# Kernel optimization log

Measured on AMD Instinct MI355X. Metric: run time of the kernel, lower is better.

## Reference

```python
import jax, jax.numpy as jnp
import numpy as np

EPS = 1e-12  # torch F.normalize eps


def setup_inputs() -> dict:
    key = jax.random.key(0)
    k1, k2, k3, k4, k5 = jax.random.split(key, 5)
    N, C, H, W = 32, 512, 32, 32
    E = 1024   # expansion * dim
    G = 8      # group
    D = E // G # 128, per-group channel dim
    K = 64     # num_clusters
    x = jax.random.normal(k1, (N, C, H, W), dtype=jnp.float32)
    W1 = jax.random.normal(k2, (E, C), dtype=jnp.float32) / np.sqrt(C)
    W2 = jax.random.normal(k3, (G, E), dtype=jnp.float32) / np.sqrt(E)
    Wc = jax.random.normal(k4, (K, D), dtype=jnp.float32) / np.sqrt(D)
    centroids = jax.random.uniform(k5, (K, D), dtype=jnp.float32)
    return {"x": x, "W1": W1, "W2": W2, "Wc": Wc, "centroids": centroids}


def reference(x, W1, W2, Wc, centroids):
    # x: [N, C, H, W]; W1: [E, C]; W2: [G, E]; Wc: [K, D]; centroids: [K, D]
    N, C, H, W = x.shape
    E = W1.shape[0]
    G = W2.shape[0]
    K, D = Wc.shape
    P = H * W
    # descriptor-wise L2 normalization over channel dim
    norm = jnp.linalg.norm(x, axis=1, keepdims=True)
    x = x / jnp.maximum(norm, EPS)
    # linear1 on channels: [N, E, P]
    xe = jnp.einsum('ncp,ec->nep', x.reshape(N, C, P), W1)
    # grouped features: [N, G, D, P]
    xg = xe.reshape(N, G, D, P)
    # attention gate: sigmoid(linear2)  -> [N, G, P]
    att = jax.nn.sigmoid(jnp.einsum('nep,ge->ngp', xe, W2))
    # 1x1 conv = per-pixel matmul with cluster weights -> [N, G, K, P]
    soft_assign = jax.nn.softmax(jnp.einsum('ngdp,kd->ngkp', xg, Wc), axis=2)
    # combined per-(cluster,pixel) weight
    w = soft_assign * att[:, :, None, :]  # [N, G, K, P]
    # NetVLAD residual aggregation, algebraically decomposed to avoid the
    # giant [N,G,K,D,P] intermediate:
    #   vlad[n,k,d] = sum_{g,p} w * xg  -  centroids[k,d] * sum_{g,p} w
    agg = jnp.einsum('ngkp,ngdp->nkd', w, xg)  # [N, K, D]
    wsum = w.sum(axis=(1, 3))                  # [N, K]
    vlad = agg - wsum[:, :, None] * centroids[None]  # [N, K, D]
    return vlad.reshape(N, K * D)
```

## Files before the change

### kernel.cpp

```cpp
#include <hip/hip_runtime.h>


#define N_  32
#define C_  512
#define P_  1024
#define E_  1024
#define G_  8
#define D_  128
#define K_  64

typedef __attribute__((ext_vector_type(8))) short bf16x8;
typedef __attribute__((ext_vector_type(4))) float f32x4;

__device__ __forceinline__ unsigned short f2b(float f) {
    union { float f; unsigned u; } v; v.f = f;
    unsigned r = (v.u + 0x7FFFu + ((v.u >> 16) & 1u)) >> 16;
    return (unsigned short)r;
}
__device__ __forceinline__ float b2f(unsigned short h) {
    union { unsigned u; float f; } v; v.u = ((unsigned)h) << 16;
    return v.f;
}

__device__ __forceinline__ void gl_lds16(const void* g, void* l) {
    __builtin_amdgcn_global_load_lds(
        (const __attribute__((address_space(1))) void*)g,
        (__attribute__((address_space(3))) void*)l, 16, 0, 0);
}

__global__ __launch_bounds__(256) void k1_norm_prep(const float* __restrict__ x,
                                                    const float* __restrict__ W1,
                                                    const float* __restrict__ Wc,
                                                    unsigned short* __restrict__ xhat_t,
                                                    unsigned short* __restrict__ W1b,
                                                    unsigned short* __restrict__ Vb) {
    __shared__ short xc[128 * 256];
    __shared__ float red[256];
    __shared__ float rn[64];
    int t = threadIdx.x;

    if (blockIdx.x >= 16) {
        int bid = (blockIdx.x - 16) * 32 + blockIdx.y;
        int i0 = bid * 512 + t;
        W1b[i0]       = f2b(W1[i0]);
        W1b[i0 + 256] = f2b(W1[i0 + 256]);
        int ch = bid & 1, k = (bid >> 1) & 63, g = bid >> 7;
        int c = ch * 256 + t;
        float acc = 0.f;
        #pragma unroll 8
        for (int d = 0; d < 128; ++d)
            acc += Wc[k * 128 + d] * W1[(g * 128 + d) * C_ + c];
        Vb[(g * 64 + k) * C_ + c] = f2b(acc);
        return;
    }

    int n = blockIdx.y;
    int p0 = blockIdx.x * 64;
    int ps = t & 63, cs = t >> 6;

    float ss = 0.f;
    for (int i = 0; i < 128; ++i) {
        float v = x[((size_t)(n * C_ + cs * 128 + i)) * P_ + p0 + ps];
        ss += v * v;
        xc[i * 256 + t] = (short)f2b(v);
    }
    red[t] = ss;
    __syncthreads();
    if (t < 64) {
        float s = red[t] + red[64 + t] + red[128 + t] + red[192 + t];
        rn[t] = 1.0f / fmaxf(sqrtf(s), 1e-12f);
    }
    __syncthreads();

    float r = rn[ps];
    size_t base = ((size_t)(n * P_ + p0 + ps)) * C_ + cs * 128;
    #pragma unroll
    for (int jj = 0; jj < 16; ++jj) {
        bf16x8 o;
        #pragma unroll
        for (int j = 0; j < 8; ++j)
            o[j] = (short)f2b(b2f((unsigned short)xc[(jj * 8 + j) * 256 + t]) * r);
        *(bf16x8*)&xhat_t[base + jj * 8] = o;
    }
}

__global__ __launch_bounds__(256) void k2_gemm_xe(const unsigned short* __restrict__ W1b,
                                                  const unsigned short* __restrict__ xhat_t,
                                                  unsigned short* __restrict__ xe) {
    __shared__ __align__(16) short As[128 * 32];
    __shared__ __align__(16) short Bs[128 * 32];
    int n = blockIdx.y;
    int e0 = (blockIdx.x >> 3) * 128;
    int p0 = (blockIdx.x & 7) * 128;
    int t = threadIdx.x;
    int w = t >> 6, l = t & 63, q = l >> 4, l15 = l & 15;
    int wr = w >> 1, wc = w & 1;

    f32x4 acc[4][4];
    #pragma unroll
    for (int mi = 0; mi < 4; ++mi)
        #pragma unroll
        for (int ni = 0; ni < 4; ++ni)
            acc[mi][ni] = (f32x4){0.f, 0.f, 0.f, 0.f};

    for (int ks = 0; ks < 16; ++ks) {
        int k0 = ks * 32;
        #pragma unroll
        for (int i = 0; i < 2; ++i) {
            int ch = i * 256 + t;
            int row = ch >> 2, col = (ch & 3) * 8;
            gl_lds16(&W1b[(e0 + row) * C_ + k0 + col], &As[ch * 8]);
        }
        #pragma unroll
        for (int i = 0; i < 2; ++i) {
            int ch = i * 256 + t;
            int row = ch >> 2, col = (ch & 3) * 8;
            gl_lds16(&xhat_t[((size_t)(n * P_ + p0 + row)) * C_ + k0 + col], &Bs[ch * 8]);
        }
        __syncthreads();

        bf16x8 af[4], bf[4];
        #pragma unroll
        for (int mi = 0; mi < 4; ++mi)
            af[mi] = *(const bf16x8*)&As[(wr * 64 + mi * 16 + l15) * 32 + q * 8];
        #pragma unroll
        for (int ni = 0; ni < 4; ++ni)
            bf[ni] = *(const bf16x8*)&Bs[(wc * 64 + ni * 16 + l15) * 32 + q * 8];
        #pragma unroll
        for (int mi = 0; mi < 4; ++mi)
            #pragma unroll
            for (int ni = 0; ni < 4; ++ni)
                acc[mi][ni] = __builtin_amdgcn_mfma_f32_16x16x32_bf16(af[mi], bf[ni], acc[mi][ni], 0, 0, 0);
        __syncthreads();
    }

    #pragma unroll
    for (int mi = 0; mi < 4; ++mi) {
        #pragma unroll
        for (int ni = 0; ni < 4; ++ni) {
            #pragma unroll
            for (int r = 0; r < 4; ++r) {
                int e = e0 + wr * 64 + mi * 16 + q * 4 + r;
                int p = p0 + wc * 64 + ni * 16 + l15;
                xe[((size_t)(n * E_ + e)) * P_ + p] = f2b(acc[mi][ni][r]);
            }
        }
    }
}

__global__ __launch_bounds__(256) void k3a_att_part(const unsigned short* __restrict__ xe,
                                                    const float* __restrict__ W2,
                                                    float* __restrict__ att_part) {
    int n = blockIdx.y;
    int ec = blockIdx.x;
    int t = threadIdx.x;
    int e0 = ec * 64;
    f32x4 acc[8];
    #pragma unroll
    for (int g = 0; g < 8; ++g) acc[g] = (f32x4){0.f, 0.f, 0.f, 0.f};
    #pragma unroll 4
    for (int i = 0; i < 64; ++i) {
        int e = e0 + i;
        ushort4 v4 = *(const ushort4*)&xe[((size_t)(n * E_ + e)) * P_ + t * 4];
        f32x4 vf = {b2f(v4.x), b2f(v4.y), b2f(v4.z), b2f(v4.w)};
        #pragma unroll
        for (int g = 0; g < 8; ++g)
            acc[g] += vf * W2[g * E_ + e];
    }
    #pragma unroll
    for (int g = 0; g < 8; ++g)
        *(f32x4*)&att_part[(((size_t)(n * 16 + ec)) * 8 + g) * P_ + t * 4] = acc[g];
}

__global__ __launch_bounds__(256) void k3b_att_reduce(const float* __restrict__ att_part,
                                                      float* __restrict__ att_s) {
    int idx = blockIdx.x * 256 + threadIdx.x;
    int p = idx & 1023;
    int g = (idx >> 10) & 7;
    int n = idx >> 13;
    float s = 0.f;
    #pragma unroll
    for (int ec = 0; ec < 16; ++ec)
        s += att_part[(((size_t)(n * 16 + ec)) * 8 + g) * P_ + p];
    att_s[idx] = 1.0f / (1.0f + __expf(-s));
}

__global__ __launch_bounds__(256) void k4_assign_agg(const unsigned short* __restrict__ Vb,
                                                     const unsigned short* __restrict__ xhat_t,
                                                     const unsigned short* __restrict__ xe,
                                                     const float* __restrict__ att_s,
                                                     float* __restrict__ agg_part,
                                                     float* __restrict__ wsum_part) {
    __shared__ __align__(16) char smem[34816 + 17408];
    short* xglds = (short*)smem;
    short* As2   = (short*)smem;
    short* Bs2   = (short*)(smem + 4096);
    short* wlds  = (short*)(smem + 34816);

    int g = blockIdx.x & 7, ph = blockIdx.x >> 3, n = blockIdx.y;
    int t = threadIdx.x;
    int w = t >> 6, l = t & 63, q = l >> 4, l15 = l & 15;

    f32x4 acc_a[4][2];
    #pragma unroll
    for (int mi = 0; mi < 4; ++mi)
        #pragma unroll
        for (int ni = 0; ni < 2; ++ni)
            acc_a[mi][ni] = (f32x4){0.f, 0.f, 0.f, 0.f};
    float wsp[16];
    #pragma unroll
    for (int j = 0; j < 16; ++j) wsp[j] = 0.f;

    for (int cc = 0; cc < 4; ++cc) {
        int p0c = ph * 512 + cc * 128;

        f32x4 acc_s[4][2];
        #pragma unroll
        for (int mi = 0; mi < 4; ++mi)
            #pragma unroll
            for (int ni = 0; ni < 2; ++ni)
                acc_s[mi][ni] = (f32x4){0.f, 0.f, 0.f, 0.f};

        for (int ks = 0; ks < 16; ++ks) {
            int k0 = ks * 32;
            {
                int row = t >> 2, col = (t & 3) * 8;
                gl_lds16(&Vb[(g * 64 + row) * C_ + k0 + col], &As2[t * 8]);
            }
            #pragma unroll
            for (int i = 0; i < 2; ++i) {
                int ch = i * 256 + t;
                int row = ch >> 2, col = (ch & 3) * 8;
                gl_lds16(&xhat_t[((size_t)(n * P_ + p0c + row)) * C_ + k0 + col], &Bs2[ch * 8]);
            }
            __syncthreads();
            bf16x8 af[4], bf2[2];
            #pragma unroll
            for (int mi = 0; mi < 4; ++mi)
                af[mi] = *(const bf16x8*)&As2[(mi * 16 + l15) * 32 + q * 8];
            #pragma unroll
            for (int ni = 0; ni < 2; ++ni)
                bf2[ni] = *(const bf16x8*)&Bs2[(w * 32 + ni * 16 + l15) * 32 + q * 8];
            #pragma unroll
            for (int mi = 0; mi < 4; ++mi)
                #pragma unroll
                for (int ni = 0; ni < 2; ++ni)
                    acc_s[mi][ni] = __builtin_amdgcn_mfma_f32_16x16x32_bf16(af[mi], bf2[ni], acc_s[mi][ni], 0, 0, 0);
            __syncthreads();
        }

        #pragma unroll
        for (int ni = 0; ni < 2; ++ni) {
            float m = -1e30f;
            #pragma unroll
            for (int mi = 0; mi < 4; ++mi)
                #pragma unroll
                for (int r = 0; r < 4; ++r)
                    m = fmaxf(m, acc_s[mi][ni][r]);
            m = fmaxf(m, __shfl_xor(m, 16));
            m = fmaxf(m, __shfl_xor(m, 32));
            float s = 0.f;
            #pragma unroll
            for (int mi = 0; mi < 4; ++mi)
                #pragma unroll
                for (int r = 0; r < 4; ++r) {
                    float e = __expf(acc_s[mi][ni][r] - m);
                    acc_s[mi][ni][r] = e;
                    s += e;
                }
            s += __shfl_xor(s, 16);
            s += __shfl_xor(s, 32);

            int pcol = p0c + w * 32 + ni * 16 + l15;
            float av = att_s[(((size_t)(n * G_ + g)) * P_) + pcol];
            float scale = av / s;

            #pragma unroll
            for (int mi = 0; mi < 4; ++mi)
                #pragma unroll
                for (int r = 0; r < 4; ++r) {
                    float wv = acc_s[mi][ni][r] * scale;
                    wsp[mi * 4 + r] += wv;
                    wlds[(mi * 16 + q * 4 + r) * 136 + (w * 32 + ni * 16 + l15)] = (short)f2b(wv);
                }
        }

        #pragma unroll
        for (int i = 0; i < 8; ++i) {
            int ch = i * 256 + t;
            int row = ch / 17, col = (ch % 17) * 8;
            gl_lds16(&xe[((size_t)(n * E_ + g * 128 + row)) * P_ + p0c + col], &xglds[ch * 8]);
        }
        if (t < 128) {
            int ch = 2048 + t;
            int row = ch / 17, col = (ch % 17) * 8;
            gl_lds16(&xe[((size_t)(n * E_ + g * 128 + row)) * P_ + p0c + col], &xglds[ch * 8]);
        }
        __syncthreads();

        #pragma unroll
        for (int pk = 0; pk < 4; ++pk) {
            bf16x8 a2[4], b2[2];
            #pragma unroll
            for (int mi = 0; mi < 4; ++mi)
                a2[mi] = *(const bf16x8*)&wlds[(mi * 16 + l15) * 136 + pk * 32 + q * 8];
            #pragma unroll
            for (int ni = 0; ni < 2; ++ni)
                b2[ni] = *(const bf16x8*)&xglds[(w * 32 + ni * 16 + l15) * 136 + pk * 32 + q * 8];
            #pragma unroll
            for (int mi = 0; mi < 4; ++mi)
                #pragma unroll
                for (int ni = 0; ni < 2; ++ni)
                    acc_a[mi][ni] = __builtin_amdgcn_mfma_f32_16x16x32_bf16(a2[mi], b2[ni], acc_a[mi][ni], 0, 0, 0);
        }
        __syncthreads();
    }

    size_t base = (((size_t)(n * G_ + g)) * 2 + ph) * 64;
    #pragma unroll
    for (int mi = 0; mi < 4; ++mi)
        #pragma unroll
        for (int ni = 0; ni < 2; ++ni)
            #pragma unroll
            for (int r = 0; r < 4; ++r) {
                int k = mi * 16 + q * 4 + r;
                int d = w * 32 + ni * 16 + l15;
                agg_part[(base + k) * 128 + d] = acc_a[mi][ni][r];
            }

    #pragma unroll
    for (int j = 0; j < 16; ++j) {
        float v = wsp[j];
        v += __shfl_xor(v, 1);
        v += __shfl_xor(v, 2);
        v += __shfl_xor(v, 4);
        v += __shfl_xor(v, 8);
        if (l15 == 0) {
            int k = (j >> 2) * 16 + q * 4 + (j & 3);
            wsum_part[((((size_t)(n * G_ + g)) * 2 + ph) * 4 + w) * 64 + k] = v;
        }
    }
}

__global__ __launch_bounds__(256) void k5_final(const float* __restrict__ agg_part,
                                                const float* __restrict__ wsum_part,
                                                const float* __restrict__ centroids,
                                                float* __restrict__ out) {
    int idx = blockIdx.x * 256 + threadIdx.x;
    int d = idx & 127;
    int k = (idx >> 7) & 63;
    int n = idx >> 13;
    float ws = 0.f;
    #pragma unroll
    for (int g = 0; g < 8; ++g)
        #pragma unroll
        for (int ph = 0; ph < 2; ++ph)
            #pragma unroll
            for (int w2 = 0; w2 < 4; ++w2)
                ws += wsum_part[((((size_t)(n * G_ + g)) * 2 + ph) * 4 + w2) * 64 + k];
    float agg = 0.f;
    #pragma unroll
    for (int g = 0; g < 8; ++g)
        #pragma unroll
        for (int ph = 0; ph < 2; ++ph)
            agg += agg_part[(((((size_t)(n * G_ + g)) * 2 + ph) * 64) + k) * 128 + d];
    out[idx] = agg - ws * centroids[k * 128 + d];
}

extern "C" void kernel_launch(void* const* d_in, const int* in_sizes, int n_in,
                              void* d_out, int out_size, void* d_ws, size_t ws_size,
                              hipStream_t stream) {
    const float* x         = (const float*)d_in[0];
    const float* W1        = (const float*)d_in[1];
    const float* W2        = (const float*)d_in[2];
    const float* Wc        = (const float*)d_in[3];
    const float* centroids = (const float*)d_in[4];
    float* out = (float*)d_out;

    char* ws = (char*)d_ws;
    unsigned short* W1b      = (unsigned short*)(ws + 0);
    unsigned short* Vb       = (unsigned short*)(ws + 1048576);
    unsigned short* xhat_t   = (unsigned short*)(ws + 1572864);
    unsigned short* xe       = (unsigned short*)(ws + 35127296);
    float*          att_s    = (float*)(ws + 102236160);
    float*          att_part = (float*)(ws + 103284736);
    float*          agg_part = (float*)(ws + 103284736);
    float*          wsum_part= (float*)(ws + 120061952);

    hipLaunchKernelGGL(k1_norm_prep,   dim3(48, 32), dim3(256), 0, stream,
                       x, W1, Wc, xhat_t, W1b, Vb);
    hipLaunchKernelGGL(k2_gemm_xe,     dim3(64, 32), dim3(256), 0, stream, W1b, xhat_t, xe);
    hipLaunchKernelGGL(k3a_att_part,   dim3(16, 32), dim3(256), 0, stream, xe, W2, att_part);
    hipLaunchKernelGGL(k3b_att_reduce, dim3(1024), dim3(256), 0, stream, att_part, att_s);
    hipLaunchKernelGGL(k4_assign_agg,  dim3(16, 32), dim3(256), 0, stream, Vb, xhat_t, xe,
                       att_s, agg_part, wsum_part);
    hipLaunchKernelGGL(k5_final,       dim3(1024), dim3(256), 0, stream,
                       agg_part, wsum_part, centroids, out);
}
```

Baseline: 262.7 us.

## Double K-step width in GEMMs, prefetch xe early, split prep kernel

The GEMM k2 and the assignment GEMM in k4 now stage 64-wide K slices per iteration instead of 32, which halves the number of barrier pairs and global-to-LDS rounds. In k4 the xe tile load is issued at the start of each pixel chunk into its own LDS region, so it overlaps the score GEMM and softmax instead of running after them. The weight prep (W1 cast and the Vb product) moves into a separate kernel so the normalization kernel no longer carries divergent block roles. In exchange LDS use per block grows, especially in k4, which may lower occupancy, and there is one extra kernel launch.

```diff
diff --git a/kernel.cpp b/kernel.cpp
--- a/kernel.cpp
+++ b/kernel.cpp
@@ -28,34 +28,32 @@
         (__attribute__((address_space(3))) void*)l, 16, 0, 0);
 }
 
-__global__ __launch_bounds__(256) void k1_norm_prep(const float* __restrict__ x,
-                                                    const float* __restrict__ W1,
-                                                    const float* __restrict__ Wc,
-                                                    unsigned short* __restrict__ xhat_t,
-                                                    unsigned short* __restrict__ W1b,
-                                                    unsigned short* __restrict__ Vb) {
+__global__ __launch_bounds__(256) void k0_prep(const float* __restrict__ W1,
+                                               const float* __restrict__ Wc,
+                                               unsigned short* __restrict__ W1b,
+                                               unsigned short* __restrict__ Vb) {
+    int bid = blockIdx.x;
+    int t = threadIdx.x;
+    int i0 = bid * 512 + t;
+    W1b[i0]       = f2b(W1[i0]);
+    W1b[i0 + 256] = f2b(W1[i0 + 256]);
+    int ch = bid & 1, k = (bid >> 1) & 63, g = bid >> 7;
+    int c = ch * 256 + t;
+    float acc = 0.f;
+    #pragma unroll 8
+    for (int d = 0; d < 128; ++d)
+        acc += Wc[k * 128 + d] * W1[(g * 128 + d) * C_ + c];
+    Vb[(g * 64 + k) * C_ + c] = f2b(acc);
+}
+
+__global__ __launch_bounds__(256) void k1_norm_transpose(const float* __restrict__ x,
+                                                         unsigned short* __restrict__ xhat_t) {
     __shared__ short xc[128 * 256];
     __shared__ float red[256];
     __shared__ float rn[64];
-    int t = threadIdx.x;
-
-    if (blockIdx.x >= 16) {
-        int bid = (blockIdx.x - 16) * 32 + blockIdx.y;
-        int i0 = bid * 512 + t;
-        W1b[i0]       = f2b(W1[i0]);
-        W1b[i0 + 256] = f2b(W1[i0 + 256]);
-        int ch = bid & 1, k = (bid >> 1) & 63, g = bid >> 7;
-        int c = ch * 256 + t;
-        float acc = 0.f;
-        #pragma unroll 8
-        for (int d = 0; d < 128; ++d)
-            acc += Wc[k * 128 + d] * W1[(g * 128 + d) * C_ + c];
-        Vb[(g * 64 + k) * C_ + c] = f2b(acc);
-        return;
-    }
-
     int n = blockIdx.y;
     int p0 = blockIdx.x * 64;
+    int t = threadIdx.x;
     int ps = t & 63, cs = t >> 6;
 
     float ss = 0.f;
@@ -87,8 +85,8 @@
 __global__ __launch_bounds__(256) void k2_gemm_xe(const unsigned short* __restrict__ W1b,
                                                   const unsigned short* __restrict__ xhat_t,
                                                   unsigned short* __restrict__ xe) {
-    __shared__ __align__(16) short As[128 * 32];
-    __shared__ __align__(16) short Bs[128 * 32];
+    __shared__ __align__(16) short As[128 * 64];
+    __shared__ __align__(16) short Bs[128 * 64];
     int n = blockIdx.y;
     int e0 = (blockIdx.x >> 3) * 128;
     int p0 = (blockIdx.x & 7) * 128;
@@ -103,34 +101,37 @@
         for (int ni = 0; ni < 4; ++ni)
             acc[mi][ni] = (f32x4){0.f, 0.f, 0.f, 0.f};
 
-    for (int ks = 0; ks < 16; ++ks) {
-        int k0 = ks * 32;
-        #pragma unroll
-        for (int i = 0; i < 2; ++i) {
+    for (int ks = 0; ks < 8; ++ks) {
+        int k0 = ks * 64;
+        #pragma unroll
+        for (int i = 0; i < 4; ++i) {
             int ch = i * 256 + t;
-            int row = ch >> 2, col = (ch & 3) * 8;
+            int row = ch >> 3, col = (ch & 7) * 8;
             gl_lds16(&W1b[(e0 + row) * C_ + k0 + col], &As[ch * 8]);
         }
         #pragma unroll
-        for (int i = 0; i < 2; ++i) {
+        for (int i = 0; i < 4; ++i) {
             int ch = i * 256 + t;
-            int row = ch >> 2, col = (ch & 3) * 8;
+            int row = ch >> 3, col = (ch & 7) * 8;
             gl_lds16(&xhat_t[((size_t)(n * P_ + p0 + row)) * C_ + k0 + col], &Bs[ch * 8]);
         }
         __syncthreads();
 
-        bf16x8 af[4], bf[4];
-        #pragma unroll
-        for (int mi = 0; mi < 4; ++mi)
-            af[mi] = *(const bf16x8*)&As[(wr * 64 + mi * 16 + l15) * 32 + q * 8];
-        #pragma unroll
-        for (int ni = 0; ni < 4; ++ni)
-            bf[ni] = *(const bf16x8*)&Bs[(wc * 64 + ni * 16 + l15) * 32 + q * 8];
-        #pragma unroll
-        for (int mi = 0; mi < 4; ++mi)
+        #pragma unroll
+        for (int kk = 0; kk < 2; ++kk) {
+            bf16x8 af[4], bf[4];
+            #pragma unroll
+            for (int mi = 0; mi < 4; ++mi)
+                af[mi] = *(const bf16x8*)&As[(wr * 64 + mi * 16 + l15) * 64 + kk * 32 + q * 8];
             #pragma unroll
             for (int ni = 0; ni < 4; ++ni)
-                acc[mi][ni] = __builtin_amdgcn_mfma_f32_16x16x32_bf16(af[mi], bf[ni], acc[mi][ni], 0, 0, 0);
+                bf[ni] = *(const bf16x8*)&Bs[(wc * 64 + ni * 16 + l15) * 64 + kk * 32 + q * 8];
+            #pragma unroll
+            for (int mi = 0; mi < 4; ++mi)
+                #pragma unroll
+                for (int ni = 0; ni < 4; ++ni)
+                    acc[mi][ni] = __builtin_amdgcn_mfma_f32_16x16x32_bf16(af[mi], bf[ni], acc[mi][ni], 0, 0, 0);
+        }
         __syncthreads();
     }
 
@@ -191,11 +192,11 @@
                                                      const float* __restrict__ att_s,
                                                      float* __restrict__ agg_part,
                                                      float* __restrict__ wsum_part) {
-    __shared__ __align__(16) char smem[34816 + 17408];
-    short* xglds = (short*)smem;
+    __shared__ __align__(16) char smem[8192 + 16384 + 34816 + 17408];
     short* As2   = (short*)smem;
-    short* Bs2   = (short*)(smem + 4096);
-    short* wlds  = (short*)(smem + 34816);
+    short* Bs2   = (short*)(smem + 8192);
+    short* xglds = (short*)(smem + 24576);
+    short* wlds  = (short*)(smem + 59392);
 
     int g = blockIdx.x & 7, ph = blockIdx.x >> 3, n = blockIdx.y;
     int t = threadIdx.x;
@@ -214,6 +215,18 @@
     for (int cc = 0; cc < 4; ++cc) {
         int p0c = ph * 512 + cc * 128;
 
+        #pragma unroll
+        for (int i = 0; i < 8; ++i) {
+            int ch = i * 256 + t;
+            int row = ch / 17, col = (ch % 17) * 8;
+            gl_lds16(&xe[((size_t)(n * E_ + g * 128 + row)) * P_ + p0c + col], &xglds[ch * 8]);
+        }
+        if (t < 128) {
+            int ch = 2048 + t;
+            int row = ch / 17, col = (ch % 17) * 8;
+            gl_lds16(&xe[((size_t)(n * E_ + g * 128 + row)) * P_ + p0c + col], &xglds[ch * 8]);
+        }
+
         f32x4 acc_s[4][2];
         #pragma unroll
         for (int mi = 0; mi < 4; ++mi)
@@ -221,31 +234,36 @@
             for (int ni = 0; ni < 2; ++ni)
                 acc_s[mi][ni] = (f32x4){0.f, 0.f, 0.f, 0.f};
 
-        for (int ks = 0; ks < 16; ++ks) {
-            int k0 = ks * 32;
-            {
-                int row = t >> 2, col = (t & 3) * 8;
-                gl_lds16(&Vb[(g * 64 + row) * C_ + k0 + col], &As2[t * 8]);
-            }
+        for (int ks = 0; ks < 8; ++ks) {
+            int k0 = ks * 64;
             #pragma unroll
             for (int i = 0; i < 2; ++i) {
                 int ch = i * 256 + t;
-                int row = ch >> 2, col = (ch & 3) * 8;
+                int row = ch >> 3, col = (ch & 7) * 8;
+                gl_lds16(&Vb[(g * 64 + row) * C_ + k0 + col], &As2[ch * 8]);
+            }
+            #pragma unroll
+            for (int i = 0; i < 4; ++i) {
+                int ch = i * 256 + t;
+                int row = ch >> 3, col = (ch & 7) * 8;
                 gl_lds16(&xhat_t[((size_t)(n * P_ + p0c + row)) * C_ + k0 + col], &Bs2[ch * 8]);
             }
             __syncthreads();
-            bf16x8 af[4], bf2[2];
-            #pragma unroll
-            for (int mi = 0; mi < 4; ++mi)
-                af[mi] = *(const bf16x8*)&As2[(mi * 16 + l15) * 32 + q * 8];
-            #pragma unroll
-            for (int ni = 0; ni < 2; ++ni)
-                bf2[ni] = *(const bf16x8*)&Bs2[(w * 32 + ni * 16 + l15) * 32 + q * 8];
-            #pragma unroll
-            for (int mi = 0; mi < 4; ++mi)
+            #pragma unroll
+            for (int kk = 0; kk < 2; ++kk) {
+                bf16x8 af[4], bf2[2];
+                #pragma unroll
+                for (int mi = 0; mi < 4; ++mi)
+                    af[mi] = *(const bf16x8*)&As2[(mi * 16 + l15) * 64 + kk * 32 + q * 8];
                 #pragma unroll
                 for (int ni = 0; ni < 2; ++ni)
-                    acc_s[mi][ni] = __builtin_amdgcn_mfma_f32_16x16x32_bf16(af[mi], bf2[ni], acc_s[mi][ni], 0, 0, 0);
+                    bf2[ni] = *(const bf16x8*)&Bs2[(w * 32 + ni * 16 + l15) * 64 + kk * 32 + q * 8];
+                #pragma unroll
+                for (int mi = 0; mi < 4; ++mi)
+                    #pragma unroll
+                    for (int ni = 0; ni < 2; ++ni)
+                        acc_s[mi][ni] = __builtin_amdgcn_mfma_f32_16x16x32_bf16(af[mi], bf2[ni], acc_s[mi][ni], 0, 0, 0);
+            }
             __syncthreads();
         }
 
@@ -283,18 +301,6 @@
                     wsp[mi * 4 + r] += wv;
                     wlds[(mi * 16 + q * 4 + r) * 136 + (w * 32 + ni * 16 + l15)] = (short)f2b(wv);
                 }
-        }
-
-        #pragma unroll
-        for (int i = 0; i < 8; ++i) {
-            int ch = i * 256 + t;
-            int row = ch / 17, col = (ch % 17) * 8;
-            gl_lds16(&xe[((size_t)(n * E_ + g * 128 + row)) * P_ + p0c + col], &xglds[ch * 8]);
-        }
-        if (t < 128) {
-            int ch = 2048 + t;
-            int row = ch / 17, col = (ch % 17) * 8;
-            gl_lds16(&xe[((size_t)(n * E_ + g * 128 + row)) * P_ + p0c + col], &xglds[ch * 8]);
         }
         __syncthreads();
 
@@ -387,8 +393,8 @@
     float*          agg_part = (float*)(ws + 103284736);
     float*          wsum_part= (float*)(ws + 120061952);
 
-    hipLaunchKernelGGL(k1_norm_prep,   dim3(48, 32), dim3(256), 0, stream,
-                       x, W1, Wc, xhat_t, W1b, Vb);
+    hipLaunchKernelGGL(k0_prep,        dim3(1024), dim3(256), 0, stream, W1, Wc, W1b, Vb);
+    hipLaunchKernelGGL(k1_norm_transpose, dim3(16, 32), dim3(256), 0, stream, x, xhat_t);
     hipLaunchKernelGGL(k2_gemm_xe,     dim3(64, 32), dim3(256), 0, stream, W1b, xhat_t, xe);
     hipLaunchKernelGGL(k3a_att_part,   dim3(16, 32), dim3(256), 0, stream, xe, W2, att_part);
     hipLaunchKernelGGL(k3b_att_reduce, dim3(1024), dim3(256), 0, stream, att_part, att_s);
```

New measurement: 253.6 us. 3.5% less time.
